# Performance work log

Hardware: AMD Instinct MI355X
Metric: run time of the kernel (lower is better)

## Reference

```python
import jax, jax.numpy as jnp
import numpy as np

CUTOFF = 5.0
MAX_NUM_PAIRS = 131072
N_ATOMS = 4096
BOX_L = 40.0


def setup_inputs() -> dict:
    key = jax.random.key(0)
    k1, _ = jax.random.split(key)
    positions = jax.random.uniform(k1, (N_ATOMS, 3), dtype=jnp.float32) * BOX_L
    box = jnp.eye(3, dtype=jnp.float32) * BOX_L  # triclinic box vectors (rows)
    return {"positions": positions, "box": box}


def _min_image_deltas(positions, box):
    # delta[i, j] = positions[i] - positions[j], wrapped by the minimum image
    # convention: subtract the nearest integer multiple of the box vectors.
    delta = positions[:, None, :] - positions[None, :, :]  # [N, N, 3]
    inv_box = jnp.linalg.inv(box)
    frac = delta @ inv_box                                  # fractional coords
    delta = delta - jnp.round(frac) @ box
    return delta


def reference(positions, box):
    n = positions.shape[0]
    delta = _min_image_deltas(positions, box)               # [N, N, 3]
    dist2 = jnp.sum(delta * delta, axis=-1)                 # [N, N]

    idx = jnp.arange(n)
    upper = idx[:, None] < idx[None, :]                     # unique pairs i<j
    mask = upper & (dist2 < CUTOFF * CUTOFF)

    n_pairs = jnp.sum(mask).astype(jnp.int32)
    # Compact hit pairs into a fixed-size buffer (static shape for jit).
    flat_idx, = jnp.nonzero(mask.ravel(), size=MAX_NUM_PAIRS, fill_value=0)
    valid = jnp.arange(MAX_NUM_PAIRS) < n_pairs

    pair_i = jnp.where(valid, flat_idx // n, -1)
    pair_j = jnp.where(valid, flat_idx % n, -1)
    pairs = jnp.stack([pair_i, pair_j], axis=0)             # [2, P]

    deltas = jnp.where(valid[:, None], delta.reshape(n * n, 3)[flat_idx], 0.0)
    d2 = jnp.where(valid, dist2.ravel()[flat_idx], 1.0)     # safe sqrt on pads
    distances = jnp.where(valid, jnp.sqrt(d2), 0.0)

    return pairs, deltas, distances, n_pairs
```

## Files before the change

### kernel.cpp

```cpp
#include <hip/hip_runtime.h>


#define CUT2 25.0f

__device__ __forceinline__ void load_box_inv(const float* __restrict__ box,
                                             float B[3][3], float Binv[3][3]) {
    #pragma unroll
    for (int r = 0; r < 3; ++r)
        #pragma unroll
        for (int c = 0; c < 3; ++c)
            B[r][c] = box[r * 3 + c];

    float a00 = B[0][0], a01 = B[0][1], a02 = B[0][2];
    float a10 = B[1][0], a11 = B[1][1], a12 = B[1][2];
    float a20 = B[2][0], a21 = B[2][1], a22 = B[2][2];

    float adj00 =  (a11 * a22 - a12 * a21);
    float adj01 = -(a01 * a22 - a02 * a21);
    float adj02 =  (a01 * a12 - a02 * a11);
    float adj10 = -(a10 * a22 - a12 * a20);
    float adj11 =  (a00 * a22 - a02 * a20);
    float adj12 = -(a00 * a12 - a02 * a10);
    float adj20 =  (a10 * a21 - a11 * a20);
    float adj21 = -(a00 * a21 - a01 * a20);
    float adj22 =  (a00 * a11 - a01 * a10);

    float det = a00 * adj00 + a01 * adj10 + a02 * adj20;

    Binv[0][0] = __fdiv_rn(adj00, det); Binv[0][1] = __fdiv_rn(adj01, det); Binv[0][2] = __fdiv_rn(adj02, det);
    Binv[1][0] = __fdiv_rn(adj10, det); Binv[1][1] = __fdiv_rn(adj11, det); Binv[1][2] = __fdiv_rn(adj12, det);
    Binv[2][0] = __fdiv_rn(adj20, det); Binv[2][1] = __fdiv_rn(adj21, det); Binv[2][2] = __fdiv_rn(adj22, det);
}

__device__ __forceinline__ void min_image(float xi, float yi, float zi,
                                          float xj, float yj, float zj,
                                          const float B[3][3], const float Binv[3][3],
                                          float& dx, float& dy, float& dz, float& d2) {
    dx = __fsub_rn(xi, xj);
    dy = __fsub_rn(yi, yj);
    dz = __fsub_rn(zi, zj);

    float f0 = __fadd_rn(__fadd_rn(__fmul_rn(dx, Binv[0][0]), __fmul_rn(dy, Binv[1][0])), __fmul_rn(dz, Binv[2][0]));
    float f1 = __fadd_rn(__fadd_rn(__fmul_rn(dx, Binv[0][1]), __fmul_rn(dy, Binv[1][1])), __fmul_rn(dz, Binv[2][1]));
    float f2 = __fadd_rn(__fadd_rn(__fmul_rn(dx, Binv[0][2]), __fmul_rn(dy, Binv[1][2])), __fmul_rn(dz, Binv[2][2]));

    float r0 = rintf(f0), r1 = rintf(f1), r2 = rintf(f2);

    float c0 = __fadd_rn(__fadd_rn(__fmul_rn(r0, B[0][0]), __fmul_rn(r1, B[1][0])), __fmul_rn(r2, B[2][0]));
    float c1 = __fadd_rn(__fadd_rn(__fmul_rn(r0, B[0][1]), __fmul_rn(r1, B[1][1])), __fmul_rn(r2, B[2][1]));
    float c2 = __fadd_rn(__fadd_rn(__fmul_rn(r0, B[0][2]), __fmul_rn(r1, B[1][2])), __fmul_rn(r2, B[2][2]));

    dx = __fsub_rn(dx, c0);
    dy = __fsub_rn(dy, c1);
    dz = __fsub_rn(dz, c2);

    d2 = __fadd_rn(__fadd_rn(__fmul_rn(dx, dx), __fmul_rn(dy, dy)), __fmul_rn(dz, dz));
}

__global__ void pad_out_kernel(float* __restrict__ out, int P) {
    int total = 6 * P + 1;
    for (int idx = blockIdx.x * blockDim.x + threadIdx.x; idx < total;
         idx += gridDim.x * blockDim.x) {
        out[idx] = (idx < 2 * P) ? -1.0f : 0.0f;
    }
}

__global__ void count_rows_kernel(const float* __restrict__ pos, const float* __restrict__ box,
                                  int* __restrict__ counts, int N) {
    int gwave = (blockIdx.x * blockDim.x + threadIdx.x) >> 6;
    int lane = threadIdx.x & 63;
    if (gwave >= N) return;
    int i = gwave;

    float B[3][3], Binv[3][3];
    load_box_inv(box, B, Binv);

    float xi = pos[3 * i + 0], yi = pos[3 * i + 1], zi = pos[3 * i + 2];

    int cnt = 0;
    int jb0 = (i >> 6) << 6;
    for (int jb = jb0; jb < N; jb += 64) {
        int j = jb + lane;
        bool hit = false;
        if (j > i && j < N) {
            float dx, dy, dz, d2;
            min_image(xi, yi, zi, pos[3 * j + 0], pos[3 * j + 1], pos[3 * j + 2],
                      B, Binv, dx, dy, dz, d2);
            hit = (d2 < CUT2);
        }
        unsigned long long m = __ballot(hit);
        cnt += __popcll(m);
    }
    if (lane == 0) counts[i] = cnt;
}

__global__ void scan_counts_kernel(const int* __restrict__ counts, int* __restrict__ offsets,
                                   float* __restrict__ out_npairs, int N) {
    __shared__ int s[1024];
    int tid = threadIdx.x;
    int nper = (N + 1023) / 1024;

    int v[8];
    int sum = 0;
    for (int r = 0; r < nper; ++r) {
        int k = tid * nper + r;
        v[r] = (k < N) ? counts[k] : 0;
        sum += v[r];
    }
    s[tid] = sum;
    __syncthreads();

    for (int off = 1; off < 1024; off <<= 1) {
        int t = (tid >= off) ? s[tid - off] : 0;
        __syncthreads();
        s[tid] += t;
        __syncthreads();
    }

    int run = (tid == 0) ? 0 : s[tid - 1];
    for (int r = 0; r < nper; ++r) {
        int k = tid * nper + r;
        if (k < N) offsets[k] = run;
        run += v[r];
    }
    if (tid == 1023) *out_npairs = (float)s[1023];
}

__global__ void fill_rows_kernel(const float* __restrict__ pos, const float* __restrict__ box,
                                 const int* __restrict__ offsets,
                                 float* __restrict__ out, int N, int P) {
    int gwave = (blockIdx.x * blockDim.x + threadIdx.x) >> 6;
    int lane = threadIdx.x & 63;
    if (gwave >= N) return;
    int i = gwave;

    float B[3][3], Binv[3][3];
    load_box_inv(box, B, Binv);

    float xi = pos[3 * i + 0], yi = pos[3 * i + 1], zi = pos[3 * i + 2];

    int base = offsets[i];
    int jb0 = (i >> 6) << 6;
    for (int jb = jb0; jb < N; jb += 64) {
        int j = jb + lane;
        bool hit = false;
        float dx = 0.f, dy = 0.f, dz = 0.f, d2 = 0.f;
        if (j > i && j < N) {
            min_image(xi, yi, zi, pos[3 * j + 0], pos[3 * j + 1], pos[3 * j + 2],
                      B, Binv, dx, dy, dz, d2);
            hit = (d2 < CUT2);
        }
        unsigned long long m = __ballot(hit);
        int my_pos = __popcll(m & ((1ull << lane) - 1ull));
        int slot = base + my_pos;
        if (hit && slot < P) {
            out[slot] = (float)i;
            out[P + slot] = (float)j;
            size_t db = 2 * (size_t)P + 3 * (size_t)slot;
            out[db + 0] = dx;
            out[db + 1] = dy;
            out[db + 2] = dz;
            out[5 * (size_t)P + slot] = sqrtf(d2);
        }
        base += __popcll(m);
    }
}

extern "C" void kernel_launch(void* const* d_in, const int* in_sizes, int n_in,
                              void* d_out, int out_size, void* d_ws, size_t ws_size,
                              hipStream_t stream) {
    const float* pos = (const float*)d_in[0];
    const float* box = (const float*)d_in[1];
    float* out = (float*)d_out;

    int N = in_sizes[0] / 3;
    int P = (out_size - 1) / 6;

    int* counts = (int*)d_ws;
    int* offsets = counts + N;

    int total_out = 6 * P + 1;
    int pad_blocks = (total_out + 255) / 256;
    pad_out_kernel<<<pad_blocks, 256, 0, stream>>>(out, P);

    int row_threads = N * 64;
    int row_blocks = (row_threads + 255) / 256;
    count_rows_kernel<<<row_blocks, 256, 0, stream>>>(pos, box, counts, N);

    scan_counts_kernel<<<1, 1024, 0, stream>>>(counts, offsets, out + 6 * (size_t)P, N);

    fill_rows_kernel<<<row_blocks, 256, 0, stream>>>(pos, box, offsets, out, N, P);
}
```

Baseline: 103.0 us.

## Store per-row hit bitmasks in count pass and reuse them in fill pass

```diff
diff --git a/kernel.cpp b/kernel.cpp
--- a/kernel.cpp
+++ b/kernel.cpp
@@ -57,16 +57,19 @@
     d2 = __fadd_rn(__fadd_rn(__fmul_rn(dx, dx), __fmul_rn(dy, dy)), __fmul_rn(dz, dz));
 }
 
-__global__ void pad_out_kernel(float* __restrict__ out, int P) {
+__global__ void prep_kernel(const float* __restrict__ pos, float4* __restrict__ pos4,
+                            float* __restrict__ out, int N, int P) {
+    int idx = blockIdx.x * blockDim.x + threadIdx.x;
     int total = 6 * P + 1;
-    for (int idx = blockIdx.x * blockDim.x + threadIdx.x; idx < total;
-         idx += gridDim.x * blockDim.x) {
-        out[idx] = (idx < 2 * P) ? -1.0f : 0.0f;
-    }
-}
-
-__global__ void count_rows_kernel(const float* __restrict__ pos, const float* __restrict__ box,
-                                  int* __restrict__ counts, int N) {
+    for (int k = idx; k < total; k += gridDim.x * blockDim.x)
+        out[k] = (k < 2 * P) ? -1.0f : 0.0f;
+    if (idx < N)
+        pos4[idx] = make_float4(pos[3 * idx], pos[3 * idx + 1], pos[3 * idx + 2], 0.0f);
+}
+
+__global__ void count_rows_kernel(const float4* __restrict__ pos4, const float* __restrict__ box,
+                                  int* __restrict__ counts, unsigned long long* __restrict__ masks,
+                                  int N) {
     int gwave = (blockIdx.x * blockDim.x + threadIdx.x) >> 6;
     int lane = threadIdx.x & 63;
     if (gwave >= N) return;
@@ -75,94 +78,120 @@
     float B[3][3], Binv[3][3];
     load_box_inv(box, B, Binv);
 
-    float xi = pos[3 * i + 0], yi = pos[3 * i + 1], zi = pos[3 * i + 2];
+    float4 pi = pos4[i];
+    int nchunks = N >> 6;
+    int c0 = i >> 6;
+    unsigned long long* mrow = masks + (size_t)i * nchunks;
 
     int cnt = 0;
-    int jb0 = (i >> 6) << 6;
-    for (int jb = jb0; jb < N; jb += 64) {
-        int j = jb + lane;
+
+    {
+        int j = (c0 << 6) + lane;
         bool hit = false;
-        if (j > i && j < N) {
+        if (j > i) {
+            float4 pj = pos4[j];
             float dx, dy, dz, d2;
-            min_image(xi, yi, zi, pos[3 * j + 0], pos[3 * j + 1], pos[3 * j + 2],
-                      B, Binv, dx, dy, dz, d2);
+            min_image(pi.x, pi.y, pi.z, pj.x, pj.y, pj.z, B, Binv, dx, dy, dz, d2);
             hit = (d2 < CUT2);
         }
         unsigned long long m = __ballot(hit);
+        if (lane == 0) mrow[c0] = m;
         cnt += __popcll(m);
     }
+
+    int c = c0 + 1;
+    for (; c + 2 <= nchunks; c += 2) {
+        int j0 = (c << 6) + lane;
+        float4 pj0 = pos4[j0];
+        float4 pj1 = pos4[j0 + 64];
+        float dx0, dy0, dz0, d20, dx1, dy1, dz1, d21;
+        min_image(pi.x, pi.y, pi.z, pj0.x, pj0.y, pj0.z, B, Binv, dx0, dy0, dz0, d20);
+        min_image(pi.x, pi.y, pi.z, pj1.x, pj1.y, pj1.z, B, Binv, dx1, dy1, dz1, d21);
+        unsigned long long m0 = __ballot(d20 < CUT2);
+        unsigned long long m1 = __ballot(d21 < CUT2);
+        if (lane == 0) { mrow[c] = m0; mrow[c + 1] = m1; }
+        cnt += __popcll(m0) + __popcll(m1);
+    }
+    if (c < nchunks) {
+        int j = (c << 6) + lane;
+        float4 pj = pos4[j];
+        float dx, dy, dz, d2;
+        min_image(pi.x, pi.y, pi.z, pj.x, pj.y, pj.z, B, Binv, dx, dy, dz, d2);
+        unsigned long long m = __ballot(d2 < CUT2);
+        if (lane == 0) mrow[c] = m;
+        cnt += __popcll(m);
+    }
+
     if (lane == 0) counts[i] = cnt;
 }
 
-__global__ void scan_counts_kernel(const int* __restrict__ counts, int* __restrict__ offsets,
-                                   float* __restrict__ out_npairs, int N) {
-    __shared__ int s[1024];
-    int tid = threadIdx.x;
-    int nper = (N + 1023) / 1024;
-
-    int v[8];
+__global__ void scan_kernel(const int* __restrict__ counts, int* __restrict__ offsets,
+                            float* __restrict__ out_npairs, int N) {
+    int lane = threadIdx.x;
+    int per = N >> 6;
+    int base_idx = lane * per;
+
     int sum = 0;
-    for (int r = 0; r < nper; ++r) {
-        int k = tid * nper + r;
-        v[r] = (k < N) ? counts[k] : 0;
-        sum += v[r];
-    }
-    s[tid] = sum;
-    __syncthreads();
-
-    for (int off = 1; off < 1024; off <<= 1) {
-        int t = (tid >= off) ? s[tid - off] : 0;
-        __syncthreads();
-        s[tid] += t;
-        __syncthreads();
-    }
-
-    int run = (tid == 0) ? 0 : s[tid - 1];
-    for (int r = 0; r < nper; ++r) {
-        int k = tid * nper + r;
-        if (k < N) offsets[k] = run;
-        run += v[r];
-    }
-    if (tid == 1023) *out_npairs = (float)s[1023];
-}
-
-__global__ void fill_rows_kernel(const float* __restrict__ pos, const float* __restrict__ box,
+    for (int r = 0; r < per; ++r) sum += counts[base_idx + r];
+
+    int incl = sum;
+    #pragma unroll
+    for (int d = 1; d < 64; d <<= 1) {
+        int t = __shfl_up(incl, d);
+        if (lane >= d) incl += t;
+    }
+    int run = incl - sum;
+
+    for (int r = 0; r < per; ++r) {
+        int cv = counts[base_idx + r];
+        offsets[base_idx + r] = run;
+        run += cv;
+    }
+    if (lane == 63) *out_npairs = (float)incl;
+}
+
+__global__ void fill_rows_kernel(const float4* __restrict__ pos4, const float* __restrict__ box,
                                  const int* __restrict__ offsets,
+                                 const unsigned long long* __restrict__ masks,
                                  float* __restrict__ out, int N, int P) {
     int gwave = (blockIdx.x * blockDim.x + threadIdx.x) >> 6;
     int lane = threadIdx.x & 63;
     if (gwave >= N) return;
     int i = gwave;
 
+    int nchunks = N >> 6;
+    int c0 = i >> 6;
+
+    unsigned long long mymask = masks[(size_t)i * nchunks + lane];
+    if (lane < c0) mymask = 0ull;
+
     float B[3][3], Binv[3][3];
     load_box_inv(box, B, Binv);
-
-    float xi = pos[3 * i + 0], yi = pos[3 * i + 1], zi = pos[3 * i + 2];
+    float4 pi = pos4[i];
 
     int base = offsets[i];
-    int jb0 = (i >> 6) << 6;
-    for (int jb = jb0; jb < N; jb += 64) {
-        int j = jb + lane;
-        bool hit = false;
-        float dx = 0.f, dy = 0.f, dz = 0.f, d2 = 0.f;
-        if (j > i && j < N) {
-            min_image(xi, yi, zi, pos[3 * j + 0], pos[3 * j + 1], pos[3 * j + 2],
-                      B, Binv, dx, dy, dz, d2);
-            hit = (d2 < CUT2);
+    for (int c = c0; c < nchunks; ++c) {
+        unsigned long long m = __shfl(mymask, c);
+        if (m != 0ull) {
+            bool hit = (m >> lane) & 1ull;
+            if (hit) {
+                int j = (c << 6) + lane;
+                float4 pj = pos4[j];
+                float dx, dy, dz, d2;
+                min_image(pi.x, pi.y, pi.z, pj.x, pj.y, pj.z, B, Binv, dx, dy, dz, d2);
+                int slot = base + __popcll(m & ((1ull << lane) - 1ull));
+                if (slot < P) {
+                    out[slot] = (float)i;
+                    out[P + slot] = (float)j;
+                    size_t db = 2 * (size_t)P + 3 * (size_t)slot;
+                    out[db + 0] = dx;
+                    out[db + 1] = dy;
+                    out[db + 2] = dz;
+                    out[5 * (size_t)P + slot] = sqrtf(d2);
+                }
+            }
+            base += __popcll(m);
         }
-        unsigned long long m = __ballot(hit);
-        int my_pos = __popcll(m & ((1ull << lane) - 1ull));
-        int slot = base + my_pos;
-        if (hit && slot < P) {
-            out[slot] = (float)i;
-            out[P + slot] = (float)j;
-            size_t db = 2 * (size_t)P + 3 * (size_t)slot;
-            out[db + 0] = dx;
-            out[db + 1] = dy;
-            out[db + 2] = dz;
-            out[5 * (size_t)P + slot] = sqrtf(d2);
-        }
-        base += __popcll(m);
     }
 }
 
@@ -175,19 +204,23 @@
 
     int N = in_sizes[0] / 3;
     int P = (out_size - 1) / 6;
-
-    int* counts = (int*)d_ws;
-    int* offsets = counts + N;
+    int nchunks = N >> 6;
+
+    char* w = (char*)d_ws;
+    int* counts = (int*)w;                         w += (size_t)N * sizeof(int);
+    int* offsets = (int*)w;                        w += (size_t)N * sizeof(int);
+    float4* pos4 = (float4*)w;                     w += (size_t)N * sizeof(float4);
+    unsigned long long* masks = (unsigned long long*)w;
 
     int total_out = 6 * P + 1;
     int pad_blocks = (total_out + 255) / 256;
-    pad_out_kernel<<<pad_blocks, 256, 0, stream>>>(out, P);
+    prep_kernel<<<pad_blocks, 256, 0, stream>>>(pos, pos4, out, N, P);
 
     int row_threads = N * 64;
     int row_blocks = (row_threads + 255) / 256;
-    count_rows_kernel<<<row_blocks, 256, 0, stream>>>(pos, box, counts, N);
-
-    scan_counts_kernel<<<1, 1024, 0, stream>>>(counts, offsets, out + 6 * (size_t)P, N);
-
-    fill_rows_kernel<<<row_blocks, 256, 0, stream>>>(pos, box, offsets, out, N, P);
-}
+    count_rows_kernel<<<row_blocks, 256, 0, stream>>>(pos4, box, counts, masks, N);
+
+    scan_kernel<<<1, 64, 0, stream>>>(counts, offsets, out + 6 * (size_t)P, N);
+
+    fill_rows_kernel<<<row_blocks, 256, 0, stream>>>(pos4, box, offsets, masks, out, N, P);
+}
```

Result: no change. 101.2 us (-1.7%).
